# Kernel tuning notes

Hardware: AMD Instinct MI355X
Metric: run time of the kernel (lower is better)

Reference implementation:

```python
import jax, jax.numpy as jnp
import numpy as np

IGNORE = 255
THRESH = 0.7
MIN_KEPT = 100000
AUX_W = 1.0


def resize_bilinear_ac(x, oh, ow):
    # F.interpolate(..., mode='bilinear', align_corners=True); x: (b,c,h,w)
    b, c, h, w = x.shape
    ys = jnp.linspace(0.0, h - 1.0, oh)
    xs = jnp.linspace(0.0, w - 1.0, ow)
    y0 = jnp.floor(ys).astype(jnp.int32)
    x0 = jnp.floor(xs).astype(jnp.int32)
    y1 = jnp.minimum(y0 + 1, h - 1)
    x1 = jnp.minimum(x0 + 1, w - 1)
    wy = (ys - y0)[:, None]          # (oh,1) broadcasts over (b,c,oh,w)
    wx = xs - x0                     # (ow,)
    rows = x[:, :, y0, :] * (1.0 - wy) + x[:, :, y1, :] * wy   # (b,c,oh,w)
    return rows[:, :, :, x0] * (1.0 - wx) + rows[:, :, :, x1] * wx


def ohem_ce(pred, target):
    # pred: (b,c,h,w) logits, target: (b,h,w) int labels
    b, c, h, w = pred.shape
    n = b * h * w
    t = target.reshape(-1)
    valid = t != IGNORE
    t_cl = jnp.where(valid, t, 0)
    logits = pred.transpose(0, 2, 3, 1).reshape(n, c)
    logp = jax.nn.log_softmax(logits, axis=-1)
    pix = jnp.arange(n)
    logp_t = logp[pix, t_cl]
    # prob at target class; invalid pixels filled with 1 (as in masked_fill_)
    mask_prob = jnp.where(valid, jnp.exp(logp_t), 1.0)
    idx = min(n, MIN_KEPT) - 1
    thr = jnp.maximum(jnp.asarray(THRESH, pred.dtype), jnp.sort(mask_prob)[idx])
    kept = mask_prob <= thr
    final_valid = valid & kept
    nll = -logp_t
    denom = jnp.maximum(final_valid.sum(), 1).astype(pred.dtype)
    return jnp.sum(jnp.where(final_valid, nll, 0.0)) / denom


def boundary_bce(p, t):
    # p: (n,1,h,w) probs, t: (n,1,h,w) binary targets; per-sample pos/neg weights
    pos = jnp.sum(t == 1.0, axis=(1, 2, 3), keepdims=True).astype(p.dtype)
    neg = jnp.sum(t == 0.0, axis=(1, 2, 3), keepdims=True).astype(p.dtype)
    valid = pos + neg
    wgt = jnp.where(t == 1.0, neg / valid, jnp.where(t == 0.0, pos / valid, 0.0))
    logp = jnp.clip(jnp.log(p), -100.0)          # torch BCELoss clamps log at -100
    log1mp = jnp.clip(jnp.log(1.0 - p), -100.0)
    bce = -(t * logp + (1.0 - t) * log1mp)
    return jnp.mean(wgt * bce)


def setup_inputs() -> dict:
    key = jax.random.key(0)
    k1, k2, k3, k4, k5 = jax.random.split(key, 5)
    main_pred = jax.random.normal(k1, (4, 19, 64, 128), dtype=jnp.float32)
    coarse_pred = jax.random.normal(k2, (4, 19, 64, 128), dtype=jnp.float32)
    boundary_pred = jax.random.uniform(k3, (4, 1, 64, 128), dtype=jnp.float32)
    seg_gt = jax.random.randint(k4, (4, 512, 1024), 0, 19, dtype=jnp.int32)
    boundary_gt = jax.random.randint(k5, (4, 1, 512, 1024), 0, 2).astype(jnp.float32)
    return {"main_pred": main_pred, "coarse_pred": coarse_pred,
            "boundary_pred": boundary_pred, "seg_gt": seg_gt,
            "boundary_gt": boundary_gt}


def reference(main_pred, coarse_pred, boundary_pred, seg_gt, boundary_gt):
    h, w = seg_gt.shape[1], seg_gt.shape[2]
    main_up = resize_bilinear_ac(main_pred, h, w)
    loss = ohem_ce(main_up, seg_gt)
    coarse_up = resize_bilinear_ac(coarse_pred, h, w)
    loss = loss + AUX_W * ohem_ce(coarse_up, seg_gt)
    bound_up = resize_bilinear_ac(boundary_pred, h, w)
    loss = loss + boundary_bce(bound_up, boundary_gt)
    return loss
```

## Files before the change

### kernel.cpp

```cpp
#include <hip/hip_runtime.h>

#define NPX    2097152
#define NPX4   (NPX/4)
#define CH_STR 8192
#define IMG_STR 155648

#define OFF_CTL   (2ull*NPX*4)
#define CTL_CNT1    0
#define CTL_CNT2    2048
#define CTL_GHIST   4096
#define CTL_PPSUM   24586
#define CTL_PPCNT   28682
#define CTL_BPS     33802
#define CTL_BPC     34826

#define GRID_P1    1536u

__device__ __forceinline__ void st_dev_f(float* p, float v) {
    __hip_atomic_store(p, v, __ATOMIC_RELAXED, __HIP_MEMORY_SCOPE_AGENT);
}
__device__ __forceinline__ void st_dev_u(unsigned* p, unsigned v) {
    __hip_atomic_store(p, v, __ATOMIC_RELAXED, __HIP_MEMORY_SCOPE_AGENT);
}
__device__ __forceinline__ float ld_dev_f(const float* p) {
    return __hip_atomic_load((float*)p, __ATOMIC_RELAXED, __HIP_MEMORY_SCOPE_AGENT);
}
__device__ __forceinline__ unsigned ld_dev_u(const unsigned* p) {
    return __hip_atomic_load((unsigned*)p, __ATOMIC_RELAXED, __HIP_MEMORY_SCOPE_AGENT);
}

__device__ __attribute__((noinline)) void slow_head(
    int tid, const float* __restrict__ pred, const int* __restrict__ seg,
    unsigned* __restrict__ ghist, float2* erow,
    float* smf, unsigned* smu)
{
    int xb = tid << 2;
    float fx0 = (float)xb * (127.0f / 1023.0f);
    int X = min((int)fx0, 126);
    float wA[4], wB[4], wC[4];
#pragma unroll
    for (int dx = 0; dx < 4; ++dx) {
        float fx = (float)(xb + dx) * (127.0f / 1023.0f);
        int x0 = min((int)fx, 127);
        float wx = fx - (float)x0;
        bool sm = (x0 == X);
        wA[dx] = sm ? (1.0f - wx) : 0.0f;
        wB[dx] = sm ? wx : (1.0f - wx);
        wC[dx] = sm ? 0.0f : wx;
    }

    for (int lvl = 0; lvl < 4; ++lvl) {
        if (lvl < 3) {
            for (int i = tid; i < 4096; i += 256) ghist[i] = 0u;
        }
        __syncthreads();
        unsigned pre = (lvl == 0) ? 0u : smu[0];
        float th = smf[0];
        float fs = 0.f; unsigned ic = 0;

        for (int task = 0; task < 2048; ++task) {
            int b = task >> 9, y = task & 511;
            float fy = (float)y * (63.0f / 511.0f);
            int y0 = min((int)fy, 63);
            int y1 = min(y0 + 1, 63);
            float wy = fy - (float)y0;
            const float* r0 = pred + (size_t)b * IMG_STR + y0 * 128;
            const float* r1 = pred + (size_t)b * IMG_STR + y1 * 128;
            for (int i = tid; i < 2432; i += 256) {
                int c = i >> 7, x = i & 127;
                float v0 = r0[c * CH_STR + x];
                float v1 = r1[c * CH_STR + x];
                float e = fmaf(wy, v1 - v0, v0);
                erow[c * 128 + x].x = e;
                if (x > 0)    erow[c * 128 + x - 1].y = e;
                if (x == 127) erow[c * 128 + 127].y = e;
            }
            __syncthreads();

            int P = task * 1024 + xb;
            int4 t4 = *(const int4*)(seg + P);
            int t[4] = {t4.x, t4.y, t4.z, t4.w};

            float acc[4] = {0.f, 0.f, 0.f, 0.f};
            for (int c = 0; c < 19; ++c) {
                float2 eA = erow[c * 128 + X];
                float2 eB = erow[c * 128 + X + 1];
#pragma unroll
                for (int dx = 0; dx < 4; ++dx) {
                    float l = fmaf(eA.x, wA[dx], fmaf(eA.y, wB[dx], eB.y * wC[dx]));
                    acc[dx] += __expf(l);
                }
            }
#pragma unroll
            for (int dx = 0; dx < 4; ++dx) {
                bool valid = (t[dx] != 255);
                int tc = valid ? t[dx] : 0;
                float2 eA = erow[tc * 128 + X];
                float2 eB = erow[tc * 128 + X + 1];
                float lt = fmaf(eA.x, wA[dx], fmaf(eA.y, wB[dx], eB.y * wC[dx]));
                float ls = __logf(acc[dx]);
                float n  = ls - lt;
                float p  = fminf(__expf(-n), 1.0f);
                float pr = valid ? p : 1.0f;
                if (lvl < 3) {
                    unsigned bv = __float_as_uint(pr);
                    if (lvl == 0)      atomicAdd(&ghist[bv >> 18], 1u);
                    else if (lvl == 1) { if ((bv >> 18) == pre) atomicAdd(&ghist[(bv >> 6) & 0xFFFu], 1u); }
                    else               { if ((bv >> 6) == pre) atomicAdd(&ghist[bv & 63u], 1u); }
                } else {
                    if (valid && p <= th) { fs -= __logf(p); ic++; }
                }
            }
            __syncthreads();
        }

        if (lvl < 3) {
            if (tid == 0) {
                int bins = (lvl == 2) ? 64 : 4096;
                unsigned kr = (lvl == 0) ? 100000u : smu[1];
                unsigned acc = 0;
                for (int idx = 0; idx < bins; ++idx) {
                    unsigned c = ghist[idx];
                    if (acc < kr && kr <= acc + c) {
                        if (lvl == 0)      { smu[0] = (unsigned)idx; smu[1] = kr - acc; }
                        else if (lvl == 1) { smu[0] = (pre << 12) | (unsigned)idx; smu[1] = kr - acc; }
                        else {
                            unsigned bitsv = (pre << 6) | (unsigned)idx;
                            smf[0] = fmaxf(0.7f, __uint_as_float(bitsv));
                        }
                        break;
                    }
                    acc += c;
                }
            }
            __syncthreads();
        } else {
            for (int o = 32; o; o >>= 1) {
                fs += __shfl_down(fs, o, 64);
                ic += (unsigned)__shfl_down((int)ic, o, 64);
            }
            int wave = tid >> 6, lane = tid & 63;
            if (lane == 0) { smf[4 + wave] = fs; smu[4 + wave] = ic; }
            __syncthreads();
            if (tid == 0) {
                smf[1] = smf[4] + smf[5] + smf[6] + smf[7];
                smu[2] = smu[4] + smu[5] + smu[6] + smu[7];
            }
            __syncthreads();
        }
    }
}

__global__ __launch_bounds__(256) void fused_all(
    const float* __restrict__ mp, const float* __restrict__ cp,
    const float* __restrict__ bp, const int* __restrict__ seg,
    const float* __restrict__ bg,
    float* __restrict__ ppsum, unsigned* __restrict__ ppcnt,
    float* __restrict__ bps, unsigned* __restrict__ bpc,
    unsigned* __restrict__ cnt1, unsigned* __restrict__ cnt2,
    unsigned* __restrict__ ghist,
    float* __restrict__ out)
{
    __shared__ float2 erow[19 * 128];
    __shared__ float rf[4]; __shared__ unsigned ru[4];
    __shared__ float rf2[4]; __shared__ unsigned ru2[4];
    __shared__ unsigned amLast;
    __shared__ float Pb[4], Nb[4]; __shared__ unsigned PCb[4], NCb[4];
    __shared__ float smf[8]; __shared__ unsigned smu[8];
    int bk = blockIdx.x;
    int tid = threadIdx.x;

    if (bk < 1024) {
        int v = ((bk & 7) << 7) | (bk >> 3);
        int head = v >> 9;
        int b    = (v >> 7) & 3;
        int k    = v & 127;
        const float* pred = head ? cp : mp;

        int y0g = min((int)((float)(4 * k) * (63.0f / 511.0f)), 63);
        int row0 = y0g, row1 = min(y0g + 1, 63), row2 = min(y0g + 2, 63);

        float4 rv[3][3];
#pragma unroll
        for (int r = 0; r < 3; ++r) {
            int ry = (r == 0) ? row0 : ((r == 1) ? row1 : row2);
            const float* rp = pred + (size_t)b * IMG_STR + ry * 128;
#pragma unroll
            for (int sr = 0; sr < 3; ++sr) {
                int s = tid + (sr << 8);
                if (s < 608) {
                    int c = s >> 5, x4 = (s & 31) << 2;
                    rv[r][sr] = *(const float4*)(rp + c * CH_STR + x4);
                } else {
                    rv[r][sr] = make_float4(0.f, 0.f, 0.f, 0.f);
                }
            }
        }

        int xb = tid << 2;
        float fx0 = (float)xb * (127.0f / 1023.0f);
        int X = min((int)fx0, 126);
        float wA[4], wB[4], wC[4];
#pragma unroll
        for (int dx = 0; dx < 4; ++dx) {
            float fx = (float)(xb + dx) * (127.0f / 1023.0f);
            int x0 = min((int)fx, 127);
            float wx = fx - (float)x0;
            bool sm = (x0 == X);
            wA[dx] = sm ? (1.0f - wx) : 0.0f;
            wB[dx] = sm ? wx : (1.0f - wx);
            wC[dx] = sm ? 0.0f : wx;
        }

#pragma unroll 1
        for (int d = 0; d < 4; ++d) {
            int y = (k << 2) + d;
            int task = (b << 9) + y;
            float fy = (float)y * (63.0f / 511.0f);
            int y0 = min((int)fy, 63);
            float wy = fy - (float)y0;
            int j = y0 - y0g;

            int P = task * 1024 + xb;
            int4 t4 = *(const int4*)(seg + P);
            int t[4] = {t4.x, t4.y, t4.z, t4.w};

#pragma unroll
            for (int sr = 0; sr < 3; ++sr) {
                int s = tid + (sr << 8);
                float4 cu = (j == 0) ? rv[0][sr] : rv[1][sr];
                float4 nx = (j == 0) ? rv[1][sr] : rv[2][sr];
                float e0 = fmaf(wy, nx.x - cu.x, cu.x);
                float e1 = fmaf(wy, nx.y - cu.y, cu.y);
                float e2 = fmaf(wy, nx.z - cu.z, cu.z);
                float e3 = fmaf(wy, nx.w - cu.w, cu.w);
                float en = __shfl_down(e0, 1, 64);
                if (s < 608) {
                    int c = s >> 5, x4 = (s & 31) << 2;
                    float last = ((s & 31) == 31) ? e3 : en;
                    float4 w0 = make_float4(e0, e1, e1, e2);
                    float4 w1 = make_float4(e2, e3, e3, last);
                    *(float4*)(&erow[c * 128 + x4])     = w0;
                    *(float4*)(&erow[c * 128 + x4 + 2]) = w1;
                }
            }
            __syncthreads();

            float acc[4] = {0.f, 0.f, 0.f, 0.f};
            for (int c = 0; c < 19; ++c) {
                float2 eA = erow[c * 128 + X];
                float2 eB = erow[c * 128 + X + 1];
#pragma unroll
                for (int dx = 0; dx < 4; ++dx) {
                    float l = fmaf(eA.x, wA[dx], fmaf(eA.y, wB[dx], eB.y * wC[dx]));
                    acc[dx] += __expf(l);
                }
            }

            float fs = 0.f; unsigned ic = 0;
#pragma unroll
            for (int dx = 0; dx < 4; ++dx) {
                bool valid = (t[dx] != 255);
                int tc = valid ? t[dx] : 0;
                float2 eA = erow[tc * 128 + X];
                float2 eB = erow[tc * 128 + X + 1];
                float lt = fmaf(eA.x, wA[dx], fmaf(eA.y, wB[dx], eB.y * wC[dx]));
                float ls = __logf(acc[dx]);
                float n  = ls - lt;
                float p  = fminf(__expf(-n), 1.0f);
                if (valid && p <= 0.7f) { fs += n; ic++; }
            }

            for (int o = 32; o; o >>= 1) {
                fs += __shfl_down(fs, o, 64);
                ic += (unsigned)__shfl_down((int)ic, o, 64);
            }
            int wave = tid >> 6, lane = tid & 63;
            if (lane == 0) { rf[wave] = fs; ru[wave] = ic; }
            __syncthreads();
            if (tid == 0) {
                st_dev_f(&ppsum[head * 2048 + task], rf[0] + rf[1] + rf[2] + rf[3]);
                st_dev_u(&ppcnt[head * 2048 + task], ru[0] + ru[1] + ru[2] + ru[3]);
            }
        }
    } else {
        int bb = bk - 1024;
        int b  = bb >> 7;
        int blk = bb & 127;
        float psum = 0.f, nsum = 0.f; unsigned pc = 0, nc = 0;

        for (int g = blk * 256 + tid; g < 131072; g += 128 * 256) {
            int P = g << 2;
            int y = P >> 10, xb = P & 1023;

            float fy = (float)y * (63.0f / 511.0f);
            int y0 = min((int)fy, 63);
            int y1 = min(y0 + 1, 63);
            float wy = fy - (float)y0;

            const float* r0 = bp + b * 8192 + y0 * 128;
            const float* r1 = bp + b * 8192 + y1 * 128;
            float fx0 = (float)xb * (127.0f / 1023.0f);
            int X  = min((int)fx0, 126);
            int X2 = min(X + 2, 127);
            float c0 = r0[X], c1 = r0[X + 1], c2 = r0[X2];
            float d0 = r1[X], d1 = r1[X + 1], d2 = r1[X2];
            float e0 = fmaf(wy, d0 - c0, c0);
            float e1 = fmaf(wy, d1 - c1, c1);
            float e2 = fmaf(wy, d2 - c2, c2);

            float4 t4 = *(const float4*)(bg + (size_t)b * 524288 + P);
            float tv[4] = {t4.x, t4.y, t4.z, t4.w};

#pragma unroll
            for (int dx = 0; dx < 4; ++dx) {
                float fx = (float)(xb + dx) * (127.0f / 1023.0f);
                int x0 = min((int)fx, 127);
                int x1 = min(x0 + 1, 127);
                float wx = fx - (float)x0;
                float a0 = (x0 == X)     ? e0 : e1;
                float a1 = (x1 == X + 1) ? e1 : e2;
                float p  = fmaf(wx, a1 - a0, a0);
                bool isp = (tv[dx] == 1.0f);
                bool isn = (tv[dx] == 0.0f);
                float q = isp ? p : 1.0f - p;
                float l = fmaxf(__logf(q), -100.0f);
                if (isp) { pc++; psum -= l; }
                if (isn) { nc++; nsum -= l; }
            }
        }
        for (int o = 32; o; o >>= 1) {
            psum += __shfl_down(psum, o, 64);
            nsum += __shfl_down(nsum, o, 64);
            pc   += (unsigned)__shfl_down((int)pc, o, 64);
            nc   += (unsigned)__shfl_down((int)nc, o, 64);
        }
        int wave = tid >> 6, lane = tid & 63;
        if (lane == 0) { rf[wave] = psum; rf2[wave] = nsum; ru[wave] = pc; ru2[wave] = nc; }
        __syncthreads();
        if (tid == 0) {
            st_dev_f(&bps[2 * bb],     rf[0] + rf[1] + rf[2] + rf[3]);
            st_dev_f(&bps[2 * bb + 1], rf2[0] + rf2[1] + rf2[2] + rf2[3]);
            st_dev_u(&bpc[2 * bb],     ru[0] + ru[1] + ru[2] + ru[3]);
            st_dev_u(&bpc[2 * bb + 1], ru2[0] + ru2[1] + ru2[2] + ru2[3]);
        }
    }

    __syncthreads();
    if (tid == 0) {
        asm volatile("s_waitcnt vmcnt(0)" ::: "memory");
        unsigned last = 0u;
        unsigned o1 = __hip_atomic_fetch_add(&cnt1[(bk & 63) << 5], 1u,
                                             __ATOMIC_RELAXED, __HIP_MEMORY_SCOPE_AGENT);
        if (o1 == 23u) {
            unsigned o2 = __hip_atomic_fetch_add(cnt2, 1u,
                                                 __ATOMIC_RELAXED, __HIP_MEMORY_SCOPE_AGENT);
            last = (o2 == 63u) ? 1u : 0u;
        }
        amLast = last;
    }
    __syncthreads();
    if (!amLast) return;

    float s0 = 0.f, s1 = 0.f; unsigned c0 = 0u, c1 = 0u;
    for (int i = tid; i < 2048; i += 256) {
        s0 += ld_dev_f(&ppsum[i]);        c0 += ld_dev_u(&ppcnt[i]);
        s1 += ld_dev_f(&ppsum[2048 + i]); c1 += ld_dev_u(&ppcnt[2048 + i]);
    }
    for (int o = 32; o; o >>= 1) {
        s0 += __shfl_down(s0, o, 64); s1 += __shfl_down(s1, o, 64);
        c0 += (unsigned)__shfl_down((int)c0, o, 64);
        c1 += (unsigned)__shfl_down((int)c1, o, 64);
    }
    int wv = tid >> 6, ln = tid & 63;
    if (ln == 0) { rf[wv] = s0; rf2[wv] = s1; ru[wv] = c0; ru2[wv] = c1; }
    __syncthreads();
    float S0 = rf[0] + rf[1] + rf[2] + rf[3];
    float S1 = rf2[0] + rf2[1] + rf2[2] + rf2[3];
    unsigned C0 = ru[0] + ru[1] + ru[2] + ru[3];
    unsigned C1 = ru2[0] + ru2[1] + ru2[2] + ru2[3];
    bool done0 = (C0 >= 100000u), done1 = (C1 >= 100000u);

    float hl0, hl1;
    if (done0) {
        hl0 = S0 / fmaxf((float)C0, 1.f);
    } else {
        slow_head(tid, mp, seg, ghist, erow, smf, smu);
        hl0 = smf[1] / fmaxf((float)smu[2], 1.f);
    }
    if (done1) {
        hl1 = S1 / fmaxf((float)C1, 1.f);
    } else {
        slow_head(tid, cp, seg, ghist, erow, smf, smu);
        hl1 = smf[1] / fmaxf((float)smu[2], 1.f);
    }
    float hls = hl0 + hl1;

    {
        float*    lf = (float*)erow;
        unsigned* lu = (unsigned*)erow + 256;
        for (int b = 0; b < 4; ++b) {
            float ps = 0.f, ns = 0.f; unsigned p_c = 0, n_c = 0;
            if (tid < 128) {
                int jj = b * 128 + tid;
                ps  = ld_dev_f(&bps[2 * jj]); ns  = ld_dev_f(&bps[2 * jj + 1]);
                p_c = ld_dev_u(&bpc[2 * jj]); n_c = ld_dev_u(&bpc[2 * jj + 1]);
            }
            lf[tid] = ps; lu[tid] = p_c; __syncthreads();
            for (int o = 128; o; o >>= 1) {
                if (tid < o) { lf[tid] += lf[tid + o]; lu[tid] += lu[tid + o]; }
                __syncthreads();
            }
            if (tid == 0) { Pb[b] = lf[0]; PCb[b] = lu[0]; }
            __syncthreads();
            lf[tid] = ns; lu[tid] = n_c; __syncthreads();
            for (int o = 128; o; o >>= 1) {
                if (tid < o) { lf[tid] += lf[tid + o]; lu[tid] += lu[tid + o]; }
                __syncthreads();
            }
            if (tid == 0) { Nb[b] = lf[0]; NCb[b] = lu[0]; }
            __syncthreads();
        }
        if (tid == 0) {
            float bt = 0.f;
            for (int b = 0; b < 4; ++b) {
                float pos = (float)PCb[b], neg = (float)NCb[b];
                float val = fmaxf(pos + neg, 1.f);
                bt += (neg / val) * Pb[b] + (pos / val) * Nb[b];
            }
            out[0] = hls + bt / 2097152.0f;
        }
    }
}

extern "C" void kernel_launch(void* const* d_in, const int* in_sizes, int n_in,
                              void* d_out, int out_size, void* d_ws, size_t ws_size,
                              hipStream_t stream)
{
    const float* mp  = (const float*)d_in[0];
    const float* cp  = (const float*)d_in[1];
    const float* bp  = (const float*)d_in[2];
    const int*   seg = (const int*)d_in[3];
    const float* bg  = (const float*)d_in[4];
    float* out = (float*)d_out;

    char* ws = (char*)d_ws;
    unsigned* ctl    = (unsigned*)(ws + OFF_CTL);
    unsigned* cnt1   = ctl + CTL_CNT1;
    unsigned* cnt2   = ctl + CTL_CNT2;
    unsigned* ghist  = ctl + CTL_GHIST;
    float*    ppsum  = (float*)(ctl + CTL_PPSUM);
    unsigned* ppcnt  = ctl + CTL_PPCNT;
    float*    bps    = (float*)(ctl + CTL_BPS);
    unsigned* bpc    = ctl + CTL_BPC;

    hipMemsetAsync(ws + OFF_CTL, 0, 2052ull * 4, stream);

    fused_all<<<dim3(GRID_P1), 256, 0, stream>>>(mp, cp, bp, seg, bg,
                                                 ppsum, ppcnt, bps, bpc,
                                                 cnt1, cnt2, ghist, out);
}
```

Baseline: 113.3 us.

## Process one output row per block and write per-wave partials

Each OHEM block now handles a single upsampled row instead of four rows sharing preloaded source rows, which quadruples the number of blocks (4096 plus the boundary blocks). Per-wave partial sums are written directly by lane 0, dropping the second block-wide barrier and the cross-wave reduction. The control-buffer offsets and the last-block counter threshold are resized to match. This gains parallelism and latency hiding, but source rows are reloaded once per output row instead of being reused across four rows, and the final reduction reads four times as many partials.

```diff
diff --git a/kernel.cpp b/kernel.cpp
--- a/kernel.cpp
+++ b/kernel.cpp
@@ -9,12 +9,12 @@
 #define CTL_CNT1    0
 #define CTL_CNT2    2048
 #define CTL_GHIST   4096
-#define CTL_PPSUM   24586
-#define CTL_PPCNT   28682
-#define CTL_BPS     33802
-#define CTL_BPC     34826
-
-#define GRID_P1    1536u
+#define CTL_PPSUM   8192
+#define CTL_PPCNT   24576
+#define CTL_BPS     40960
+#define CTL_BPC     41984
+
+#define GRID_P1    4608u
 
 __device__ __forceinline__ void st_dev_f(float* p, float v) {
     __hip_atomic_store(p, v, __ATOMIC_RELAXED, __HIP_MEMORY_SCOPE_AGENT);
@@ -170,34 +170,51 @@
     int bk = blockIdx.x;
     int tid = threadIdx.x;
 
-    if (bk < 1024) {
-        int v = ((bk & 7) << 7) | (bk >> 3);
-        int head = v >> 9;
-        int b    = (v >> 7) & 3;
-        int k    = v & 127;
+    if (bk < 4096) {
+        int v = ((bk & 7) << 9) | (bk >> 3);
+        int head = v >> 11;
+        int task = v & 2047;
+        int b = task >> 9;
+        int y = task & 511;
         const float* pred = head ? cp : mp;
 
-        int y0g = min((int)((float)(4 * k) * (63.0f / 511.0f)), 63);
-        int row0 = y0g, row1 = min(y0g + 1, 63), row2 = min(y0g + 2, 63);
-
-        float4 rv[3][3];
-#pragma unroll
-        for (int r = 0; r < 3; ++r) {
-            int ry = (r == 0) ? row0 : ((r == 1) ? row1 : row2);
-            const float* rp = pred + (size_t)b * IMG_STR + ry * 128;
-#pragma unroll
-            for (int sr = 0; sr < 3; ++sr) {
-                int s = tid + (sr << 8);
-                if (s < 608) {
-                    int c = s >> 5, x4 = (s & 31) << 2;
-                    rv[r][sr] = *(const float4*)(rp + c * CH_STR + x4);
-                } else {
-                    rv[r][sr] = make_float4(0.f, 0.f, 0.f, 0.f);
-                }
-            }
-        }
+        float fy = (float)y * (63.0f / 511.0f);
+        int y0 = min((int)fy, 63);
+        int y1 = min(y0 + 1, 63);
+        float wy = fy - (float)y0;
 
         int xb = tid << 2;
+        int P = task * 1024 + xb;
+        int4 t4 = *(const int4*)(seg + P);
+        int t[4] = {t4.x, t4.y, t4.z, t4.w};
+
+        const float* r0 = pred + (size_t)b * IMG_STR + y0 * 128;
+        const float* r1 = pred + (size_t)b * IMG_STR + y1 * 128;
+#pragma unroll
+        for (int sr = 0; sr < 3; ++sr) {
+            int s = tid + (sr << 8);
+            float4 cu = make_float4(0.f, 0.f, 0.f, 0.f);
+            float4 nx = make_float4(0.f, 0.f, 0.f, 0.f);
+            int c = s >> 5, x4 = (s & 31) << 2;
+            if (s < 608) {
+                cu = *(const float4*)(r0 + c * CH_STR + x4);
+                nx = *(const float4*)(r1 + c * CH_STR + x4);
+            }
+            float e0 = fmaf(wy, nx.x - cu.x, cu.x);
+            float e1 = fmaf(wy, nx.y - cu.y, cu.y);
+            float e2 = fmaf(wy, nx.z - cu.z, cu.z);
+            float e3 = fmaf(wy, nx.w - cu.w, cu.w);
+            float en = __shfl_down(e0, 1, 64);
+            if (s < 608) {
+                float last = ((s & 31) == 31) ? e3 : en;
+                float4 w0 = make_float4(e0, e1, e1, e2);
+                float4 w1 = make_float4(e2, e3, e3, last);
+                *(float4*)(&erow[c * 128 + x4])     = w0;
+                *(float4*)(&erow[c * 128 + x4 + 2]) = w1;
+            }
+        }
+        __syncthreads();
+
         float fx0 = (float)xb * (127.0f / 1023.0f);
         int X = min((int)fx0, 126);
         float wA[4], wB[4], wC[4];
@@ -212,79 +229,44 @@
             wC[dx] = sm ? 0.0f : wx;
         }
 
-#pragma unroll 1
-        for (int d = 0; d < 4; ++d) {
-            int y = (k << 2) + d;
-            int task = (b << 9) + y;
-            float fy = (float)y * (63.0f / 511.0f);
-            int y0 = min((int)fy, 63);
-            float wy = fy - (float)y0;
-            int j = y0 - y0g;
-
-            int P = task * 1024 + xb;
-            int4 t4 = *(const int4*)(seg + P);
-            int t[4] = {t4.x, t4.y, t4.z, t4.w};
-
-#pragma unroll
-            for (int sr = 0; sr < 3; ++sr) {
-                int s = tid + (sr << 8);
-                float4 cu = (j == 0) ? rv[0][sr] : rv[1][sr];
-                float4 nx = (j == 0) ? rv[1][sr] : rv[2][sr];
-                float e0 = fmaf(wy, nx.x - cu.x, cu.x);
-                float e1 = fmaf(wy, nx.y - cu.y, cu.y);
-                float e2 = fmaf(wy, nx.z - cu.z, cu.z);
-                float e3 = fmaf(wy, nx.w - cu.w, cu.w);
-                float en = __shfl_down(e0, 1, 64);
-                if (s < 608) {
-                    int c = s >> 5, x4 = (s & 31) << 2;
-                    float last = ((s & 31) == 31) ? e3 : en;
-                    float4 w0 = make_float4(e0, e1, e1, e2);
-                    float4 w1 = make_float4(e2, e3, e3, last);
-                    *(float4*)(&erow[c * 128 + x4])     = w0;
-                    *(float4*)(&erow[c * 128 + x4 + 2]) = w1;
-                }
-            }
-            __syncthreads();
-
-            float acc[4] = {0.f, 0.f, 0.f, 0.f};
-            for (int c = 0; c < 19; ++c) {
-                float2 eA = erow[c * 128 + X];
-                float2 eB = erow[c * 128 + X + 1];
-#pragma unroll
-                for (int dx = 0; dx < 4; ++dx) {
-                    float l = fmaf(eA.x, wA[dx], fmaf(eA.y, wB[dx], eB.y * wC[dx]));
-                    acc[dx] += __expf(l);
-                }
-            }
-
-            float fs = 0.f; unsigned ic = 0;
+        float acc[4] = {0.f, 0.f, 0.f, 0.f};
+        for (int c = 0; c < 19; ++c) {
+            float2 eA = erow[c * 128 + X];
+            float2 eB = erow[c * 128 + X + 1];
 #pragma unroll
             for (int dx = 0; dx < 4; ++dx) {
-                bool valid = (t[dx] != 255);
-                int tc = valid ? t[dx] : 0;
-                float2 eA = erow[tc * 128 + X];
-                float2 eB = erow[tc * 128 + X + 1];
-                float lt = fmaf(eA.x, wA[dx], fmaf(eA.y, wB[dx], eB.y * wC[dx]));
-                float ls = __logf(acc[dx]);
-                float n  = ls - lt;
-                float p  = fminf(__expf(-n), 1.0f);
-                if (valid && p <= 0.7f) { fs += n; ic++; }
-            }
-
-            for (int o = 32; o; o >>= 1) {
-                fs += __shfl_down(fs, o, 64);
-                ic += (unsigned)__shfl_down((int)ic, o, 64);
-            }
-            int wave = tid >> 6, lane = tid & 63;
-            if (lane == 0) { rf[wave] = fs; ru[wave] = ic; }
-            __syncthreads();
-            if (tid == 0) {
-                st_dev_f(&ppsum[head * 2048 + task], rf[0] + rf[1] + rf[2] + rf[3]);
-                st_dev_u(&ppcnt[head * 2048 + task], ru[0] + ru[1] + ru[2] + ru[3]);
-            }
+                float l = fmaf(eA.x, wA[dx], fmaf(eA.y, wB[dx], eB.y * wC[dx]));
+                acc[dx] += __expf(l);
+            }
+        }
+
+        float fs = 0.f; unsigned ic = 0;
+#pragma unroll
+        for (int dx = 0; dx < 4; ++dx) {
+            bool valid = (t[dx] != 255);
+            int tc = valid ? t[dx] : 0;
+            float2 eA = erow[tc * 128 + X];
+            float2 eB = erow[tc * 128 + X + 1];
+            float lt = fmaf(eA.x, wA[dx], fmaf(eA.y, wB[dx], eB.y * wC[dx]));
+            float ls = __logf(acc[dx]);
+            float n  = ls - lt;
+            float p  = fminf(__expf(-n), 1.0f);
+            if (valid && p <= 0.7f) { fs += n; ic++; }
+        }
+
+        for (int o = 32; o; o >>= 1) {
+            fs += __shfl_down(fs, o, 64);
+            ic += (unsigned)__shfl_down((int)ic, o, 64);
+        }
+        int wave = tid >> 6, lane = tid & 63;
+        if (lane == 0) {
+            int base = (head * 2048 + task) << 2;
+            st_dev_f(&ppsum[base + wave], fs);
+            st_dev_u(&ppcnt[base + wave], ic);
+            asm volatile("s_waitcnt vmcnt(0)" ::: "memory");
         }
     } else {
-        int bb = bk - 1024;
+        int bb = bk - 4096;
         int b  = bb >> 7;
         int blk = bb & 127;
         float psum = 0.f, nsum = 0.f; unsigned pc = 0, nc = 0;
@@ -352,7 +334,7 @@
         unsigned last = 0u;
         unsigned o1 = __hip_atomic_fetch_add(&cnt1[(bk & 63) << 5], 1u,
                                              __ATOMIC_RELAXED, __HIP_MEMORY_SCOPE_AGENT);
-        if (o1 == 23u) {
+        if (o1 == 71u) {
             unsigned o2 = __hip_atomic_fetch_add(cnt2, 1u,
                                                  __ATOMIC_RELAXED, __HIP_MEMORY_SCOPE_AGENT);
             last = (o2 == 63u) ? 1u : 0u;
@@ -364,8 +346,18 @@
 
     float s0 = 0.f, s1 = 0.f; unsigned c0 = 0u, c1 = 0u;
     for (int i = tid; i < 2048; i += 256) {
-        s0 += ld_dev_f(&ppsum[i]);        c0 += ld_dev_u(&ppcnt[i]);
-        s1 += ld_dev_f(&ppsum[2048 + i]); c1 += ld_dev_u(&ppcnt[2048 + i]);
+        {
+            const float* ps = &ppsum[i << 2];
+            const unsigned* pq = &ppcnt[i << 2];
+            s0 += ld_dev_f(&ps[0]) + ld_dev_f(&ps[1]) + ld_dev_f(&ps[2]) + ld_dev_f(&ps[3]);
+            c0 += ld_dev_u(&pq[0]) + ld_dev_u(&pq[1]) + ld_dev_u(&pq[2]) + ld_dev_u(&pq[3]);
+        }
+        {
+            const float* ps = &ppsum[(2048 + i) << 2];
+            const unsigned* pq = &ppcnt[(2048 + i) << 2];
+            s1 += ld_dev_f(&ps[0]) + ld_dev_f(&ps[1]) + ld_dev_f(&ps[2]) + ld_dev_f(&ps[3]);
+            c1 += ld_dev_u(&pq[0]) + ld_dev_u(&pq[1]) + ld_dev_u(&pq[2]) + ld_dev_u(&pq[3]);
+        }
     }
     for (int o = 32; o; o >>= 1) {
         s0 += __shfl_down(s0, o, 64); s1 += __shfl_down(s1, o, 64);
```

After: 118.0 us. 1.04x slower.
